# Kernel tuning notes

Measured on AMD Instinct MI355X. Metric: run time of the kernel, lower is better.

The kernel has to match this reference:

```python
import jax, jax.numpy as jnp
import numpy as np

EPS = 1e-5

def _ln(x, g, b):
    m = x.mean(-1, keepdims=True)
    v = ((x - m) ** 2).mean(-1, keepdims=True)
    return (x - m) / jnp.sqrt(v + EPS) * g + b


def setup_inputs() -> dict:
    key = jax.random.key(0)
    B, S = 16, 512
    H, dh = 16, 64            # num_head, head_size
    D = H * dh                # 1024
    NB = 2                    # num_blocks
    L = 2                     # attention_mlp_layers
    ks = jax.random.split(key, 16)
    sc = 1.0 / np.sqrt(D)
    inp = {
        'inputs': jax.random.normal(ks[0], (B, S, D), jnp.float32),
        'Wq': jax.random.normal(ks[1], (NB, H, D, dh), jnp.float32) * sc,
        'Wk': jax.random.normal(ks[2], (NB, H, D, dh), jnp.float32) * sc,
        'Wv': jax.random.normal(ks[3], (NB, H, D, dh), jnp.float32) * sc,
        'qg': jnp.ones((NB, dh), jnp.float32), 'qb': jnp.zeros((NB, dh), jnp.float32),
        'kg': jnp.ones((NB, dh), jnp.float32), 'kb': jnp.zeros((NB, dh), jnp.float32),
        'vg': jnp.ones((NB, dh), jnp.float32), 'vb': jnp.zeros((NB, dh), jnp.float32),
        'l0g': jnp.ones((NB, D), jnp.float32), 'l0b': jnp.zeros((NB, D), jnp.float32),
        'l1g': jnp.ones((NB, D), jnp.float32), 'l1b': jnp.zeros((NB, D), jnp.float32),
        'mW': jax.random.normal(ks[4], (NB, L, D, D), jnp.float32) * sc,
        'mB': jnp.zeros((NB, L, D), jnp.float32),
    }
    return inp


def reference(inputs, Wq, Wk, Wv, qg, qb, kg, kb, vg, vb, l0g, l0b, l1g, l1b, mW, mB):
    B, S, D = inputs.shape
    NB, H, _, dh = Wq.shape
    L = mW.shape[1]
    scale = 1.0 / np.sqrt(dh)  # source divides by sqrt(value_dim/n_heads)
    x = inputs
    maps = []
    for i in range(NB):
        # per-head projections: torch repeats batch over heads then bmm with [H,D,dh]
        q = jnp.einsum('bsd,hde->bhse', x, Wq[i])
        k = jnp.einsum('bsd,hde->bhse', x, Wk[i])
        v = jnp.einsum('bsd,hde->bhse', x, Wv[i])
        qn = _ln(q, qg[i], qb[i])
        kn = _ln(k, kg[i], kb[i])
        vn = _ln(v, vg[i], vb[i])
        # NOTE: the source applies NO softmax — raw scaled scores are used.
        attn = jnp.einsum('bhse,bhte->bhst', qn, kn) * scale
        o = jnp.einsum('bhst,bhte->bhse', attn, vn)
        # torch layout is (H*B, S, S) with head-major ordering
        maps.append(jnp.transpose(attn, (1, 0, 2, 3)).reshape(H * B, S, S))
        # concat heads on last dim (head-major split/cat == bhse -> bshe reshape)
        o = jnp.transpose(o, (0, 2, 1, 3)).reshape(B, S, D)
        new = _ln(x + o, l0g[i], l0b[i])  # dropout is identity in eval
        h = new
        for l in range(L):
            h = jax.nn.relu(h @ mW[i, l] + mB[i, l])
        x = _ln(new + h, l1g[i], l1b[i])
    return x, jnp.stack(maps)
```

## Files before the change

### kernel.cpp

```cpp
#include <hip/hip_runtime.h>
#include <cstddef>
#include <cstdint>

#define B_   16
#define S_   512
#define D_   1024
#define H_   16
#define DH_  64
#define BS_  8192
#define EPS_ 1e-5f

typedef __attribute__((ext_vector_type(8))) short bf16x8;
typedef __attribute__((ext_vector_type(4))) short s16x4;
typedef __attribute__((ext_vector_type(4))) float f32x4;

__device__ __forceinline__ unsigned short f2bf(float f) {
    unsigned int u = __builtin_bit_cast(unsigned int, f);
    u = (u + 0x7FFFu + ((u >> 16) & 1u)) >> 16;
    return (unsigned short)u;
}
__device__ __forceinline__ float bf2f(unsigned short h) {
    unsigned int u = ((unsigned int)h) << 16;
    return __builtin_bit_cast(float, u);
}
__device__ __forceinline__ void splitbf(float v, short& hi, short& lo) {
    unsigned short h = f2bf(v);
    float r = v - bf2f(h);
    hi = (short)h;
    lo = (short)f2bf(r);
}

__device__ __forceinline__ void gload16(const void* g, void* l) {
    __builtin_amdgcn_global_load_lds(
        (const __attribute__((address_space(1))) unsigned int*)g,
        (__attribute__((address_space(3))) unsigned int*)l, 16, 0, 0);
}


__device__ __forceinline__ void mainloop128(
    const short* __restrict__ Ah, const short* __restrict__ Al,
    const short* __restrict__ Bh, const short* __restrict__ Bl,
    int nkt, short* lds, f32x4 acc[4][4])
{
    const int t = threadIdx.x;
    const int wid = t >> 6, lane = t & 63;
    short* LAh = lds;
    short* LAl = lds + 4096;
    short* LBh = lds + 8192;
    short* LBl = lds + 12288;
    const int fa = (wid >> 1) * 4;
    const int fb = (wid & 1) * 4;
    for (int kt = 0; kt < nkt; ++kt) {
        const size_t go = (size_t)kt * 4096 + (size_t)t * 8;
        gload16(Ah + go,        LAh + t * 8);
        gload16(Ah + go + 2048, LAh + t * 8 + 2048);
        gload16(Al + go,        LAl + t * 8);
        gload16(Al + go + 2048, LAl + t * 8 + 2048);
        gload16(Bh + go,        LBh + t * 8);
        gload16(Bh + go + 2048, LBh + t * 8 + 2048);
        gload16(Bl + go,        LBl + t * 8);
        gload16(Bl + go + 2048, LBl + t * 8 + 2048);
        asm volatile("s_waitcnt vmcnt(0)" ::: "memory");
        __syncthreads();
        bf16x8 aH[4], aL[4];
        #pragma unroll
        for (int fm = 0; fm < 4; ++fm) {
            aH[fm] = *(const bf16x8*)(LAh + (fa + fm) * 512 + lane * 8);
            aL[fm] = *(const bf16x8*)(LAl + (fa + fm) * 512 + lane * 8);
        }
        #pragma unroll
        for (int fn = 0; fn < 4; ++fn) {
            bf16x8 bH = *(const bf16x8*)(LBh + (fb + fn) * 512 + lane * 8);
            bf16x8 bL = *(const bf16x8*)(LBl + (fb + fn) * 512 + lane * 8);
            #pragma unroll
            for (int fm = 0; fm < 4; ++fm) {
                acc[fm][fn] = __builtin_amdgcn_mfma_f32_16x16x32_bf16(aH[fm], bH, acc[fm][fn], 0, 0, 0);
                acc[fm][fn] = __builtin_amdgcn_mfma_f32_16x16x32_bf16(aH[fm], bL, acc[fm][fn], 0, 0, 0);
                acc[fm][fn] = __builtin_amdgcn_mfma_f32_16x16x32_bf16(aL[fm], bH, acc[fm][fn], 0, 0, 0);
            }
        }
        __syncthreads();
    }
}

__global__ __launch_bounds__(256, 3) void proj_kernel(
    const short* __restrict__ XPh, const short* __restrict__ XPl,
    const short* __restrict__ WTh, const short* __restrict__ WTl,
    const float* __restrict__ gq, const float* __restrict__ bq,
    const float* __restrict__ gk, const float* __restrict__ bk,
    const float* __restrict__ gv, const float* __restrict__ bv,
    short* __restrict__ QPh, short* __restrict__ QPl,
    short* __restrict__ KPh, short* __restrict__ KPl,
    short* __restrict__ VPh, short* __restrict__ VPl)
{
    __shared__ __align__(16) short lds[16384];
    const int mt = blockIdx.x, nt = blockIdx.y;
    f32x4 acc[4][4] = {};
    mainloop128(XPh + (size_t)mt * 131072, XPl + (size_t)mt * 131072,
                WTh + (size_t)nt * 131072, WTl + (size_t)nt * 131072,
                32, lds, acc);
    const int t = threadIdx.x, wid = t >> 6, lane = t & 63;
    const int g = lane >> 4, li = lane & 15;
    const int wm = (wid >> 1) * 64, wn = (wid & 1) * 64;
    const int n0 = nt * 128 + wn;
    const int qkv = n0 >> 10;
    const int h = (n0 >> 6) & 15;
    const float* gam = qkv == 0 ? gq : (qkv == 1 ? gk : gv);
    const float* bet = qkv == 0 ? bq : (qkv == 1 ? bk : bv);
    float gm[4], bt[4];
    #pragma unroll
    for (int fn = 0; fn < 4; ++fn) { gm[fn] = gam[fn * 16 + li]; bt[fn] = bet[fn * 16 + li]; }
    #pragma unroll
    for (int fm = 0; fm < 4; ++fm) {
        #pragma unroll
        for (int r = 0; r < 4; ++r) {
            float s = acc[fm][0][r] + acc[fm][1][r] + acc[fm][2][r] + acc[fm][3][r];
            s += __shfl_xor(s, 1, 64); s += __shfl_xor(s, 2, 64);
            s += __shfl_xor(s, 4, 64); s += __shfl_xor(s, 8, 64);
            const float mean = s * (1.f / 64.f);
            float q = 0.f;
            #pragma unroll
            for (int fn = 0; fn < 4; ++fn) { const float d = acc[fm][fn][r] - mean; q += d * d; }
            q += __shfl_xor(q, 1, 64); q += __shfl_xor(q, 2, 64);
            q += __shfl_xor(q, 4, 64); q += __shfl_xor(q, 8, 64);
            const float rstd = rsqrtf(q * (1.f / 64.f) + EPS_);
            const int m = mt * 128 + wm + fm * 16 + g * 4 + r;
            const int b = m >> 9, srow = m & 511;
            const int z = b * 16 + h;
            #pragma unroll
            for (int fn = 0; fn < 4; ++fn) {
                const float val = (acc[fm][fn][r] - mean) * rstd * gm[fn] + bt[fn];
                short hi, lo; splitbf(val, hi, lo);
                const int e = fn * 16 + li;
                if (qkv == 2) {
                    const size_t o = (size_t)z * 32768 + (size_t)srow * 64 + e;
                    VPh[o] = hi; VPl[o] = lo;
                } else {
                    const size_t o = ((size_t)((z * 4 + (srow >> 7)) * 2 + (e >> 5))) * 4096
                                   + ((((srow >> 4) & 7) * 4 + ((e >> 3) & 3)) * 16 + (srow & 15)) * 8 + (e & 7);
                    if (qkv == 0) { QPh[o] = hi; QPl[o] = lo; }
                    else          { KPh[o] = hi; KPl[o] = lo; }
                }
            }
        }
    }
}

template<int MODE>
__global__ __launch_bounds__(256, 3) void mlp_kernel(
    const short* __restrict__ Ah, const short* __restrict__ Al,
    const short* __restrict__ Bh, const short* __restrict__ Bl,
    const float* __restrict__ bias,
    short* __restrict__ OPh, short* __restrict__ OPl,
    float* __restrict__ OF)
{
    __shared__ __align__(16) short lds[16384];
    const int mt = blockIdx.x, nt = blockIdx.y;
    f32x4 acc[4][4] = {};
    mainloop128(Ah + (size_t)mt * 131072, Al + (size_t)mt * 131072,
                Bh + (size_t)nt * 131072, Bl + (size_t)nt * 131072, 32, lds, acc);
    const int t = threadIdx.x, wid = t >> 6, lane = t & 63;
    const int g = lane >> 4, li = lane & 15;
    const int wm = (wid >> 1) * 64, wn = (wid & 1) * 64;
    float bb[4];
    #pragma unroll
    for (int fn = 0; fn < 4; ++fn) bb[fn] = bias[nt * 128 + wn + fn * 16 + li];
    #pragma unroll
    for (int fm = 0; fm < 4; ++fm) {
        #pragma unroll
        for (int r = 0; r < 4; ++r) {
            const int m = mt * 128 + wm + fm * 16 + g * 4 + r;
            #pragma unroll
            for (int fn = 0; fn < 4; ++fn) {
                const int n = nt * 128 + wn + fn * 16 + li;
                float v = acc[fm][fn][r] + bb[fn];
                v = v > 0.f ? v : 0.f;
                if (MODE == 1) {
                    short hi, lo; splitbf(v, hi, lo);
                    const size_t o = ((size_t)mt * 32 + (n >> 5)) * 4096
                                   + ((((m >> 4) & 7) * 4 + ((n >> 3) & 3)) * 16 + (m & 15)) * 8 + (n & 7);
                    OPh[o] = hi; OPl[o] = lo;
                } else {
                    OF[(size_t)m * 1024 + n] = v;
                }
            }
        }
    }
}

__global__ __launch_bounds__(256, 3) void scores_kernel(
    const short* __restrict__ QPh, const short* __restrict__ QPl,
    const short* __restrict__ KPh, const short* __restrict__ KPl,
    float* __restrict__ mapsi)
{
    __shared__ __align__(16) short lds[16384];
    const int mt = blockIdx.x, nt = blockIdx.y, z = blockIdx.z;
    f32x4 acc[4][4] = {};
    const size_t ab = (size_t)(z * 4 + mt) * 8192;
    const size_t bb2 = (size_t)(z * 4 + nt) * 8192;
    mainloop128(QPh + ab, QPl + ab, KPh + bb2, KPl + bb2, 2, lds, acc);
    const int t = threadIdx.x, wid = t >> 6, lane = t & 63;
    const int g = lane >> 4, li = lane & 15;
    const int wm = (wid >> 1) * 64, wn = (wid & 1) * 64;
    const int zp = ((z & 15) << 4) | (z >> 4);
    float* P = mapsi + (size_t)zp * (S_ * S_);
    #pragma unroll
    for (int fm = 0; fm < 4; ++fm) {
        #pragma unroll
        for (int r = 0; r < 4; ++r) {
            const int srow = mt * 128 + wm + fm * 16 + g * 4 + r;
            #pragma unroll
            for (int fn = 0; fn < 4; ++fn) {
                const int tc = nt * 128 + wn + fn * 16 + li;
                P[(size_t)srow * 512 + tc] = acc[fm][fn][r] * 0.125f;
            }
        }
    }
}

__global__ __launch_bounds__(256, 3) void o_kernel(
    const float* __restrict__ maps, const short* __restrict__ VTh,
    const short* __restrict__ VTl, float* __restrict__ O)
{
    __shared__ __align__(16) short lds[12288];
    const int bid = blockIdx.x;
    const int xcd = bid & 7, tt = bid >> 3;
    const int mt = tt & 3;
    const int z = (tt >> 2) * 8 + xcd;
    const int zp = ((z & 15) << 4) | (z >> 4);
    const float* P = maps + (size_t)zp * (S_ * S_);
    const short* Bh = VTh + (size_t)z * 32768;
    const short* Bl = VTl + (size_t)z * 32768;
    short* LAh = lds;
    short* LAl = lds + 4096;
    short* LBh = lds + 8192;
    short* LBl = lds + 10240;
    const int t = threadIdx.x, wid = t >> 6, lane = t & 63;
    const int fa = (wid >> 1) * 4, fb = (wid & 1) * 2;
    f32x4 acc[4][2] = {};
    for (int kt = 0; kt < 16; ++kt) {
        gload16(Bh + (size_t)kt * 2048 + t * 8, LBh + t * 8);
        gload16(Bl + (size_t)kt * 2048 + t * 8, LBl + t * 8);
        #pragma unroll
        for (int cc = 0; cc < 2; ++cc) {
            const int c = t + cc * 256;
            const int srow = mt * 128 + (c >> 6) * 16 + (c & 15);
            const int k0 = kt * 32 + ((c >> 4) & 3) * 8;
            const float* src = P + (size_t)srow * 512 + k0;
            const f32x4 v0 = *(const f32x4*)(src);
            const f32x4 v1 = *(const f32x4*)(src + 4);
            bf16x8 h8, l8;
            #pragma unroll
            for (int j = 0; j < 4; ++j) {
                short hi, lo;
                splitbf(v0[j], hi, lo); h8[j] = hi;     l8[j] = lo;
                splitbf(v1[j], hi, lo); h8[4 + j] = hi; l8[4 + j] = lo;
            }
            *(bf16x8*)(LAh + c * 8) = h8;
            *(bf16x8*)(LAl + c * 8) = l8;
        }
        asm volatile("s_waitcnt vmcnt(0)" ::: "memory");
        __syncthreads();
        bf16x8 aH[4], aL[4];
        #pragma unroll
        for (int fm = 0; fm < 4; ++fm) {
            aH[fm] = *(const bf16x8*)(LAh + (fa + fm) * 512 + lane * 8);
            aL[fm] = *(const bf16x8*)(LAl + (fa + fm) * 512 + lane * 8);
        }
        #pragma unroll
        for (int fn = 0; fn < 2; ++fn) {
            bf16x8 bH = *(const bf16x8*)(LBh + (fb + fn) * 512 + lane * 8);
            bf16x8 bL = *(const bf16x8*)(LBl + (fb + fn) * 512 + lane * 8);
            #pragma unroll
            for (int fm = 0; fm < 4; ++fm) {
                acc[fm][fn] = __builtin_amdgcn_mfma_f32_16x16x32_bf16(aH[fm], bH, acc[fm][fn], 0, 0, 0);
                acc[fm][fn] = __builtin_amdgcn_mfma_f32_16x16x32_bf16(aH[fm], bL, acc[fm][fn], 0, 0, 0);
                acc[fm][fn] = __builtin_amdgcn_mfma_f32_16x16x32_bf16(aL[fm], bH, acc[fm][fn], 0, 0, 0);
            }
        }
        __syncthreads();
    }
    const int b = z >> 4, h = z & 15;
    const int g = lane >> 4, li = lane & 15;
    #pragma unroll
    for (int fm = 0; fm < 4; ++fm) {
        #pragma unroll
        for (int r = 0; r < 4; ++r) {
            const int srow = mt * 128 + (wid >> 1) * 64 + fm * 16 + g * 4 + r;
            #pragma unroll
            for (int fn = 0; fn < 2; ++fn) {
                const int e = (wid & 1) * 32 + fn * 16 + li;
                O[((size_t)b * 512 + srow) * 1024 + h * 64 + e] = acc[fm][fn][r];
            }
        }
    }
}

__global__ __launch_bounds__(256) void vt_kernel(
    const short* __restrict__ VPh, const short* __restrict__ VPl,
    short* __restrict__ VTh, short* __restrict__ VTl)
{
    const int z = blockIdx.x, kt = blockIdx.y;
    __shared__ __align__(16) short Th[32][80];
    __shared__ __align__(16) short Tl[32][80];
    const int t = threadIdx.x;
    {
        const int row = t >> 3;
        const int e0 = (t & 7) * 8;
        const size_t src = (size_t)z * 32768 + (size_t)(kt * 32 + row) * 64 + e0;
        *(bf16x8*)&Th[row][e0] = *(const bf16x8*)(VPh + src);
        *(bf16x8*)&Tl[row][e0] = *(const bf16x8*)(VPl + src);
    }
    __syncthreads();
    {
        const int c = t;
        const int fn = c >> 6, kc = (c >> 4) & 3, n16 = c & 15;
        const int e = fn * 16 + n16;
        bf16x8 h8, l8;
        #pragma unroll
        for (int j = 0; j < 8; ++j) {
            h8[j] = Th[kc * 8 + j][e];
            l8[j] = Tl[kc * 8 + j][e];
        }
        const size_t o = ((size_t)z * 16 + kt) * 2048 + (size_t)c * 8;
        *(bf16x8*)(VTh + o) = h8;
        *(bf16x8*)(VTl + o) = l8;
    }
}

__global__ __launch_bounds__(256) void ln_add_kernel(
    const float* __restrict__ A, const float* __restrict__ C,
    const float* __restrict__ g, const float* __restrict__ bb,
    float* __restrict__ out, short* __restrict__ Ph, short* __restrict__ Pl)
{
    const int m = blockIdx.x;
    const int t = threadIdx.x;
    const int wave = t >> 6, lane = t & 63;
    __shared__ float red1[4];
    __shared__ float red2[4];
    const int k0 = t * 4;
    const f32x4 va = *(const f32x4*)(A + (size_t)m * 1024 + k0);
    const f32x4 vc = *(const f32x4*)(C + (size_t)m * 1024 + k0);
    f32x4 v = va + vc;
    float s = v[0] + v[1] + v[2] + v[3];
    #pragma unroll
    for (int off = 32; off > 0; off >>= 1) s += __shfl_xor(s, off, 64);
    if (lane == 0) red1[wave] = s;
    __syncthreads();
    const float mean = (red1[0] + red1[1] + red1[2] + red1[3]) * (1.f / 1024.f);
    float q = 0.f;
    #pragma unroll
    for (int j = 0; j < 4; ++j) { const float d = v[j] - mean; q += d * d; }
    #pragma unroll
    for (int off = 32; off > 0; off >>= 1) q += __shfl_xor(q, off, 64);
    if (lane == 0) red2[wave] = q;
    __syncthreads();
    const float rstd = rsqrtf((red2[0] + red2[1] + red2[2] + red2[3]) * (1.f / 1024.f) + EPS_);
    const f32x4 gg = *(const f32x4*)(g + k0);
    const f32x4 bv = *(const f32x4*)(bb + k0);
    f32x4 o;
    s16x4 hi4, lo4;
    #pragma unroll
    for (int j = 0; j < 4; ++j) {
        o[j] = (v[j] - mean) * rstd * gg[j] + bv[j];
        short hi, lo; splitbf(o[j], hi, lo);
        hi4[j] = hi; lo4[j] = lo;
    }
    *(f32x4*)(out + (size_t)m * 1024 + k0) = o;
    const size_t po = ((size_t)(m >> 7) * 32 + (k0 >> 5)) * 4096
                    + ((((m >> 4) & 7) * 4 + ((k0 >> 3) & 3)) * 16 + (m & 15)) * 8 + (k0 & 7);
    *(s16x4*)(Ph + po) = hi4;
    *(s16x4*)(Pl + po) = lo4;
}

__global__ __launch_bounds__(256) void cvt_kernel(
    const float* __restrict__ X, short* __restrict__ Ph, short* __restrict__ Pl)
{
    const int m = blockIdx.x;
    const int t = threadIdx.x;
    const int k0 = t * 4;
    const f32x4 v = *(const f32x4*)(X + (size_t)m * 1024 + k0);
    s16x4 hi4, lo4;
    #pragma unroll
    for (int j = 0; j < 4; ++j) { short hi, lo; splitbf(v[j], hi, lo); hi4[j] = hi; lo4[j] = lo; }
    const size_t po = ((size_t)(m >> 7) * 32 + (k0 >> 5)) * 4096
                    + ((((m >> 4) & 7) * 4 + ((k0 >> 3) & 3)) * 16 + (m & 15)) * 8 + (k0 & 7);
    *(s16x4*)(Ph + po) = hi4;
    *(s16x4*)(Pl + po) = lo4;
}

__global__ __launch_bounds__(256) void prep_wqkv_kernel(
    const float* __restrict__ Wq, const float* __restrict__ Wk,
    const float* __restrict__ Wv, short* __restrict__ WTh, short* __restrict__ WTl)
{
    const int nt = blockIdx.x;
    const int kt = blockIdx.y;
    const int qkv = nt >> 3;
    const float* W = qkv == 0 ? Wq : (qkv == 1 ? Wk : Wv);
    const int t = threadIdx.x;
    short* oh = WTh + ((size_t)nt * 32 + kt) * 4096;
    short* ol = WTl + ((size_t)nt * 32 + kt) * 4096;
    #pragma unroll
    for (int cc = 0; cc < 2; ++cc) {
        const int c = t + cc * 256;
        const int nloc = (c >> 6) * 16 + (c & 15);
        const int nq = (nt & 7) * 128 + nloc;
        const int h = nq >> 6, e = nq & 63;
        const int d0 = kt * 32 + ((c >> 4) & 3) * 8;
        bf16x8 h8, l8;
        #pragma unroll
        for (int j = 0; j < 8; ++j) {
            const float v = W[((size_t)h * 1024 + d0 + j) * 64 + e];
            short hi, lo; splitbf(v, hi, lo);
            h8[j] = hi; l8[j] = lo;
        }
        *(bf16x8*)(oh + c * 8) = h8;
        *(bf16x8*)(ol + c * 8) = l8;
    }
}

__global__ __launch_bounds__(256) void prep_mw_kernel(
    const float* __restrict__ Wm, short* __restrict__ Mh, short* __restrict__ Ml)
{
    const int nt = blockIdx.x;
    const int kt = blockIdx.y;
    const int l  = blockIdx.z;
    const float* W = Wm + (size_t)l * 1048576;
    short* oh = Mh + (size_t)l * 1048576 + ((size_t)nt * 32 + kt) * 4096;
    short* ol = Ml + (size_t)l * 1048576 + ((size_t)nt * 32 + kt) * 4096;
    const int t = threadIdx.x;
    #pragma unroll
    for (int cc = 0; cc < 2; ++cc) {
        const int c = t + cc * 256;
        const int n = nt * 128 + (c >> 6) * 16 + (c & 15);
        const int k0 = kt * 32 + ((c >> 4) & 3) * 8;
        bf16x8 h8, l8;
        #pragma unroll
        for (int j = 0; j < 8; ++j) {
            const float v = W[(size_t)(k0 + j) * 1024 + n];
            short hi, lo; splitbf(v, hi, lo);
            h8[j] = hi; l8[j] = lo;
        }
        *(bf16x8*)(oh + c * 8) = h8;
        *(bf16x8*)(ol + c * 8) = l8;
    }
}

extern "C" void kernel_launch(void* const* d_in, const int* in_sizes, int n_in,
                              void* d_out, int out_size, void* d_ws, size_t ws_size,
                              hipStream_t stream)
{
    const float* inputs = (const float*)d_in[0];
    const float* Wq  = (const float*)d_in[1];
    const float* Wk  = (const float*)d_in[2];
    const float* Wv  = (const float*)d_in[3];
    const float* qg  = (const float*)d_in[4];
    const float* qb  = (const float*)d_in[5];
    const float* kg  = (const float*)d_in[6];
    const float* kb  = (const float*)d_in[7];
    const float* vg  = (const float*)d_in[8];
    const float* vb  = (const float*)d_in[9];
    const float* l0g = (const float*)d_in[10];
    const float* l0b = (const float*)d_in[11];
    const float* l1g = (const float*)d_in[12];
    const float* l1b = (const float*)d_in[13];
    const float* mW  = (const float*)d_in[14];
    const float* mB  = (const float*)d_in[15];

    float* xout = (float*)d_out;
    float* maps = xout + (size_t)BS_ * D_;

    char* ws = (char*)d_ws;
    short* XPh = (short*)(ws);
    short* XPl = (short*)(ws + 16777216);
    short* QPh = (short*)(ws + 33554432);
    short* QPl = (short*)(ws + 50331648);
    short* KPh = (short*)(ws + 67108864);
    short* KPl = (short*)(ws + 83886080);
    float* NEW = (float*)(ws + 100663296);
    short* VPh = (short*)(ws + 100663296);
    short* VPl = (short*)(ws + 117440512);
    float* OF  = (float*)(ws + 134217728);
    short* WTh = (short*)(ws + 167772160);
    short* WTl = (short*)(ws + 174063616);
    short* MWh = (short*)(ws + 180355072);
    short* MWl = (short*)(ws + 184549376);
    short* VTh = XPh;
    short* VTl = XPl;

    const dim3 blk(256);
    for (int i = 0; i < 2; ++i) {
        const float* xin = (i == 0) ? inputs : xout;
        float* mapsi = maps + (size_t)i * H_ * B_ * S_ * S_;

        if (i == 0)
            cvt_kernel<<<dim3(BS_), blk, 0, stream>>>(inputs, XPh, XPl);

        prep_wqkv_kernel<<<dim3(24, 32), blk, 0, stream>>>(
            Wq + (size_t)i * H_ * D_ * DH_, Wk + (size_t)i * H_ * D_ * DH_,
            Wv + (size_t)i * H_ * D_ * DH_, WTh, WTl);
        prep_mw_kernel<<<dim3(8, 32, 2), blk, 0, stream>>>(
            mW + (size_t)i * 2 * D_ * D_, MWh, MWl);

        proj_kernel<<<dim3(64, 24), blk, 0, stream>>>(
            XPh, XPl, WTh, WTl,
            qg + i * DH_, qb + i * DH_, kg + i * DH_, kb + i * DH_,
            vg + i * DH_, vb + i * DH_,
            QPh, QPl, KPh, KPl, VPh, VPl);

        vt_kernel<<<dim3(256, 16), blk, 0, stream>>>(VPh, VPl, VTh, VTl);

        scores_kernel<<<dim3(4, 4, 256), blk, 0, stream>>>(QPh, QPl, KPh, KPl, mapsi);

        o_kernel<<<dim3(1024), blk, 0, stream>>>(mapsi, VTh, VTl, OF);

        ln_add_kernel<<<dim3(BS_), blk, 0, stream>>>(
            xin, OF, l0g + i * D_, l0b + i * D_, NEW, KPh, KPl);

        mlp_kernel<1><<<dim3(64, 8), blk, 0, stream>>>(
            KPh, KPl, MWh, MWl, mB + (size_t)(i * 2 + 0) * D_, QPh, QPl, (float*)nullptr);
        mlp_kernel<2><<<dim3(64, 8), blk, 0, stream>>>(
            QPh, QPl, MWh + 1048576, MWl + 1048576, mB + (size_t)(i * 2 + 1) * D_,
            (short*)nullptr, (short*)nullptr, OF);

        ln_add_kernel<<<dim3(BS_), blk, 0, stream>>>(
            NEW, OF, l1g + i * D_, l1b + i * D_, xout, XPh, XPl);
    }
}
```

Measured before the change: 1.576 ms.

## Compute attention output via Q(KᵀV) reassociation instead of reading score maps

Because no softmax is applied, the output is computed as Q·(KᵀV·scale) per head in a new kernel. This replaces the kernel that re-read the full fp32 score maps and multiplied them by V, removing a large memory-bound pass. The score maps are still written, now with nontemporal stores, and the maps output region serves as scratch for row-major K/V and their transposes before scores_kernel overwrites it. Projection and MLP grids are remapped to a 1D launch with an XCD-aware block swizzle. The cost is an extra K write, an extra transpose kernel and scratch aliasing that depends on the launch order.

```diff
diff --git a/kernel.cpp b/kernel.cpp
--- a/kernel.cpp
+++ b/kernel.cpp
@@ -91,10 +91,13 @@
     const float* __restrict__ gv, const float* __restrict__ bv,
     short* __restrict__ QPh, short* __restrict__ QPl,
     short* __restrict__ KPh, short* __restrict__ KPl,
-    short* __restrict__ VPh, short* __restrict__ VPl)
+    short* __restrict__ KRMh, short* __restrict__ KRMl,
+    short* __restrict__ VRMh, short* __restrict__ VRMl)
 {
     __shared__ __align__(16) short lds[16384];
-    const int mt = blockIdx.x, nt = blockIdx.y;
+    const int f  = blockIdx.x;
+    const int nf = (f & 7) * 192 + (f >> 3);
+    const int mt = nf & 63, nt = nf >> 6;
     f32x4 acc[4][4] = {};
     mainloop128(XPh + (size_t)mt * 131072, XPl + (size_t)mt * 131072,
                 WTh + (size_t)nt * 131072, WTl + (size_t)nt * 131072,
@@ -134,12 +137,16 @@
                 const int e = fn * 16 + li;
                 if (qkv == 2) {
                     const size_t o = (size_t)z * 32768 + (size_t)srow * 64 + e;
-                    VPh[o] = hi; VPl[o] = lo;
+                    VRMh[o] = hi; VRMl[o] = lo;
                 } else {
                     const size_t o = ((size_t)((z * 4 + (srow >> 7)) * 2 + (e >> 5))) * 4096
                                    + ((((srow >> 4) & 7) * 4 + ((e >> 3) & 3)) * 16 + (srow & 15)) * 8 + (e & 7);
                     if (qkv == 0) { QPh[o] = hi; QPl[o] = lo; }
-                    else          { KPh[o] = hi; KPl[o] = lo; }
+                    else {
+                        KPh[o] = hi; KPl[o] = lo;
+                        const size_t o2 = (size_t)z * 32768 + (size_t)srow * 64 + e;
+                        KRMh[o2] = hi; KRMl[o2] = lo;
+                    }
                 }
             }
         }
@@ -155,7 +162,9 @@
     float* __restrict__ OF)
 {
     __shared__ __align__(16) short lds[16384];
-    const int mt = blockIdx.x, nt = blockIdx.y;
+    const int f  = blockIdx.x;
+    const int nf = (f & 7) * 64 + (f >> 3);
+    const int mt = nf & 63, nt = nf >> 6;
     f32x4 acc[4][4] = {};
     mainloop128(Ah + (size_t)mt * 131072, Al + (size_t)mt * 131072,
                 Bh + (size_t)nt * 131072, Bl + (size_t)nt * 131072, 32, lds, acc);
@@ -212,93 +221,108 @@
             #pragma unroll
             for (int fn = 0; fn < 4; ++fn) {
                 const int tc = nt * 128 + wn + fn * 16 + li;
-                P[(size_t)srow * 512 + tc] = acc[fm][fn][r] * 0.125f;
-            }
-        }
-    }
-}
-
-__global__ __launch_bounds__(256, 3) void o_kernel(
-    const float* __restrict__ maps, const short* __restrict__ VTh,
-    const short* __restrict__ VTl, float* __restrict__ O)
-{
-    __shared__ __align__(16) short lds[12288];
-    const int bid = blockIdx.x;
-    const int xcd = bid & 7, tt = bid >> 3;
-    const int mt = tt & 3;
-    const int z = (tt >> 2) * 8 + xcd;
-    const int zp = ((z & 15) << 4) | (z >> 4);
-    const float* P = maps + (size_t)zp * (S_ * S_);
-    const short* Bh = VTh + (size_t)z * 32768;
-    const short* Bl = VTl + (size_t)z * 32768;
-    short* LAh = lds;
-    short* LAl = lds + 4096;
-    short* LBh = lds + 8192;
-    short* LBl = lds + 10240;
+                __builtin_nontemporal_store(acc[fm][fn][r] * 0.125f,
+                                            P + (size_t)srow * 512 + tc);
+            }
+        }
+    }
+}
+
+__global__ __launch_bounds__(256) void kvo2_kernel(
+    const short* __restrict__ VTKh, const short* __restrict__ VTKl,
+    const short* __restrict__ VTVh, const short* __restrict__ VTVl,
+    const short* __restrict__ QPh, const short* __restrict__ QPl,
+    float* __restrict__ O)
+{
+    __shared__ __align__(16) short kvt[8192];
+    __shared__ __align__(16) short qs[16384];
+    const int z = blockIdx.x;
     const int t = threadIdx.x, wid = t >> 6, lane = t & 63;
-    const int fa = (wid >> 1) * 4, fb = (wid & 1) * 2;
-    f32x4 acc[4][2] = {};
+    const int g = lane >> 4, li = lane & 15;
+
+    f32x4 acc[4] = {};
+    const size_t zb = (size_t)z * 32768;
     for (int kt = 0; kt < 16; ++kt) {
-        gload16(Bh + (size_t)kt * 2048 + t * 8, LBh + t * 8);
-        gload16(Bl + (size_t)kt * 2048 + t * 8, LBl + t * 8);
-        #pragma unroll
-        for (int cc = 0; cc < 2; ++cc) {
-            const int c = t + cc * 256;
-            const int srow = mt * 128 + (c >> 6) * 16 + (c & 15);
-            const int k0 = kt * 32 + ((c >> 4) & 3) * 8;
-            const float* src = P + (size_t)srow * 512 + k0;
-            const f32x4 v0 = *(const f32x4*)(src);
-            const f32x4 v1 = *(const f32x4*)(src + 4);
-            bf16x8 h8, l8;
-            #pragma unroll
-            for (int j = 0; j < 4; ++j) {
-                short hi, lo;
-                splitbf(v0[j], hi, lo); h8[j] = hi;     l8[j] = lo;
-                splitbf(v1[j], hi, lo); h8[4 + j] = hi; l8[4 + j] = lo;
-            }
-            *(bf16x8*)(LAh + c * 8) = h8;
-            *(bf16x8*)(LAl + c * 8) = l8;
-        }
+        const size_t tb = zb + (size_t)kt * 2048;
+        const bf16x8 aH = *(const bf16x8*)(VTKh + tb + wid * 512 + lane * 8);
+        const bf16x8 aL = *(const bf16x8*)(VTKl + tb + wid * 512 + lane * 8);
+        #pragma unroll
+        for (int fn = 0; fn < 4; ++fn) {
+            const bf16x8 bH = *(const bf16x8*)(VTVh + tb + fn * 512 + lane * 8);
+            const bf16x8 bL = *(const bf16x8*)(VTVl + tb + fn * 512 + lane * 8);
+            acc[fn] = __builtin_amdgcn_mfma_f32_16x16x32_bf16(aH, bH, acc[fn], 0, 0, 0);
+            acc[fn] = __builtin_amdgcn_mfma_f32_16x16x32_bf16(aH, bL, acc[fn], 0, 0, 0);
+            acc[fn] = __builtin_amdgcn_mfma_f32_16x16x32_bf16(aL, bH, acc[fn], 0, 0, 0);
+        }
+    }
+    #pragma unroll
+    for (int fn = 0; fn < 4; ++fn) {
+        #pragma unroll
+        for (int r = 0; r < 4; ++r) {
+            const int e1 = wid * 16 + g * 4 + r;
+            const int e2 = fn * 16 + li;
+            short hi, lo; splitbf(acc[fn][r] * 0.125f, hi, lo);
+            const int a = (e1 >> 5) * 2048 + (e2 >> 4) * 512
+                        + ((((e1 >> 3) & 3) * 16) + (e2 & 15)) * 8 + (e1 & 7);
+            kvt[a] = hi; kvt[4096 + a] = lo;
+        }
+    }
+    __syncthreads();
+
+    const int b = z >> 4, h = z & 15;
+    const int fa = (wid >> 1) * 4, fbn = (wid & 1) * 2;
+    for (int mt = 0; mt < 4; ++mt) {
+        __syncthreads();
+        const size_t qb = (size_t)(z * 4 + mt) * 8192;
+        gload16(QPh + qb + t * 8,        qs + t * 8);
+        gload16(QPh + qb + t * 8 + 2048, qs + t * 8 + 2048);
+        gload16(QPh + qb + t * 8 + 4096, qs + t * 8 + 4096);
+        gload16(QPh + qb + t * 8 + 6144, qs + t * 8 + 6144);
+        gload16(QPl + qb + t * 8,        qs + 8192 + t * 8);
+        gload16(QPl + qb + t * 8 + 2048, qs + 8192 + t * 8 + 2048);
+        gload16(QPl + qb + t * 8 + 4096, qs + 8192 + t * 8 + 4096);
+        gload16(QPl + qb + t * 8 + 6144, qs + 8192 + t * 8 + 6144);
         asm volatile("s_waitcnt vmcnt(0)" ::: "memory");
         __syncthreads();
-        bf16x8 aH[4], aL[4];
+        f32x4 a3[4][2] = {};
+        #pragma unroll
+        for (int kt2 = 0; kt2 < 2; ++kt2) {
+            bf16x8 aH[4], aL[4];
+            #pragma unroll
+            for (int fm = 0; fm < 4; ++fm) {
+                aH[fm] = *(const bf16x8*)(qs + kt2 * 4096 + (fa + fm) * 512 + lane * 8);
+                aL[fm] = *(const bf16x8*)(qs + 8192 + kt2 * 4096 + (fa + fm) * 512 + lane * 8);
+            }
+            #pragma unroll
+            for (int fnb = 0; fnb < 2; ++fnb) {
+                const bf16x8 bH = *(const bf16x8*)(kvt + kt2 * 2048 + (fbn + fnb) * 512 + lane * 8);
+                const bf16x8 bL = *(const bf16x8*)(kvt + 4096 + kt2 * 2048 + (fbn + fnb) * 512 + lane * 8);
+                #pragma unroll
+                for (int fm = 0; fm < 4; ++fm) {
+                    a3[fm][fnb] = __builtin_amdgcn_mfma_f32_16x16x32_bf16(aH[fm], bH, a3[fm][fnb], 0, 0, 0);
+                    a3[fm][fnb] = __builtin_amdgcn_mfma_f32_16x16x32_bf16(aH[fm], bL, a3[fm][fnb], 0, 0, 0);
+                    a3[fm][fnb] = __builtin_amdgcn_mfma_f32_16x16x32_bf16(aL[fm], bH, a3[fm][fnb], 0, 0, 0);
+                }
+            }
+        }
         #pragma unroll
         for (int fm = 0; fm < 4; ++fm) {
-            aH[fm] = *(const bf16x8*)(LAh + (fa + fm) * 512 + lane * 8);
-            aL[fm] = *(const bf16x8*)(LAl + (fa + fm) * 512 + lane * 8);
-        }
-        #pragma unroll
-        for (int fn = 0; fn < 2; ++fn) {
-            bf16x8 bH = *(const bf16x8*)(LBh + (fb + fn) * 512 + lane * 8);
-            bf16x8 bL = *(const bf16x8*)(LBl + (fb + fn) * 512 + lane * 8);
-            #pragma unroll
-            for (int fm = 0; fm < 4; ++fm) {
-                acc[fm][fn] = __builtin_amdgcn_mfma_f32_16x16x32_bf16(aH[fm], bH, acc[fm][fn], 0, 0, 0);
-                acc[fm][fn] = __builtin_amdgcn_mfma_f32_16x16x32_bf16(aH[fm], bL, acc[fm][fn], 0, 0, 0);
-                acc[fm][fn] = __builtin_amdgcn_mfma_f32_16x16x32_bf16(aL[fm], bH, acc[fm][fn], 0, 0, 0);
-            }
-        }
-        __syncthreads();
-    }
-    const int b = z >> 4, h = z & 15;
-    const int g = lane >> 4, li = lane & 15;
-    #pragma unroll
-    for (int fm = 0; fm < 4; ++fm) {
-        #pragma unroll
-        for (int r = 0; r < 4; ++r) {
-            const int srow = mt * 128 + (wid >> 1) * 64 + fm * 16 + g * 4 + r;
-            #pragma unroll
-            for (int fn = 0; fn < 2; ++fn) {
-                const int e = (wid & 1) * 32 + fn * 16 + li;
-                O[((size_t)b * 512 + srow) * 1024 + h * 64 + e] = acc[fm][fn][r];
+            #pragma unroll
+            for (int r = 0; r < 4; ++r) {
+                const int s = mt * 128 + (wid >> 1) * 64 + fm * 16 + g * 4 + r;
+                #pragma unroll
+                for (int fnb = 0; fnb < 2; ++fnb) {
+                    const int e2 = (fbn + fnb) * 16 + li;
+                    O[((size_t)b * 512 + s) * 1024 + h * 64 + e2] = a3[fm][fnb][r];
+                }
             }
         }
     }
 }
 
 __global__ __launch_bounds__(256) void vt_kernel(
-    const short* __restrict__ VPh, const short* __restrict__ VPl,
-    short* __restrict__ VTh, short* __restrict__ VTl)
+    const short* __restrict__ Sh, const short* __restrict__ Sl,
+    short* __restrict__ Dh, short* __restrict__ Dl)
 {
     const int z = blockIdx.x, kt = blockIdx.y;
     __shared__ __align__(16) short Th[32][80];
@@ -308,8 +332,8 @@
         const int row = t >> 3;
         const int e0 = (t & 7) * 8;
         const size_t src = (size_t)z * 32768 + (size_t)(kt * 32 + row) * 64 + e0;
-        *(bf16x8*)&Th[row][e0] = *(const bf16x8*)(VPh + src);
-        *(bf16x8*)&Tl[row][e0] = *(const bf16x8*)(VPl + src);
+        *(bf16x8*)&Th[row][e0] = *(const bf16x8*)(Sh + src);
+        *(bf16x8*)&Tl[row][e0] = *(const bf16x8*)(Sl + src);
     }
     __syncthreads();
     {
@@ -323,8 +347,8 @@
             l8[j] = Tl[kc * 8 + j][e];
         }
         const size_t o = ((size_t)z * 16 + kt) * 2048 + (size_t)c * 8;
-        *(bf16x8*)(VTh + o) = h8;
-        *(bf16x8*)(VTl + o) = l8;
+        *(bf16x8*)(Dh + o) = h8;
+        *(bf16x8*)(Dl + o) = l8;
     }
 }
 
@@ -478,20 +502,25 @@
     short* KPh = (short*)(ws + 67108864);
     short* KPl = (short*)(ws + 83886080);
     float* NEW = (float*)(ws + 100663296);
-    short* VPh = (short*)(ws + 100663296);
-    short* VPl = (short*)(ws + 117440512);
     float* OF  = (float*)(ws + 134217728);
     short* WTh = (short*)(ws + 167772160);
     short* WTl = (short*)(ws + 174063616);
     short* MWh = (short*)(ws + 180355072);
     short* MWl = (short*)(ws + 184549376);
-    short* VTh = XPh;
-    short* VTl = XPl;
 
     const dim3 blk(256);
     for (int i = 0; i < 2; ++i) {
         const float* xin = (i == 0) ? inputs : xout;
         float* mapsi = maps + (size_t)i * H_ * B_ * S_ * S_;
+
+        short* KRMh = (short*)mapsi;
+        short* KRMl = KRMh + 8388608;
+        short* VRMh = KRMh + 16777216;
+        short* VRMl = KRMh + 25165824;
+        short* VTKh = KRMh + 33554432;
+        short* VTKl = KRMh + 41943040;
+        short* VTVh = KRMh + 50331648;
+        short* VTVl = KRMh + 58720256;
 
         if (i == 0)
             cvt_kernel<<<dim3(BS_), blk, 0, stream>>>(inputs, XPh, XPl);
@@ -502,24 +531,26 @@
         prep_mw_kernel<<<dim3(8, 32, 2), blk, 0, stream>>>(
             mW + (size_t)i * 2 * D_ * D_, MWh, MWl);
 
-        proj_kernel<<<dim3(64, 24), blk, 0, stream>>>(
+        proj_kernel<<<dim3(1536), blk, 0, stream>>>(
             XPh, XPl, WTh, WTl,
             qg + i * DH_, qb + i * DH_, kg + i * DH_, kb + i * DH_,
             vg + i * DH_, vb + i * DH_,
-            QPh, QPl, KPh, KPl, VPh, VPl);
-
-        vt_kernel<<<dim3(256, 16), blk, 0, stream>>>(VPh, VPl, VTh, VTl);
+            QPh, QPl, KPh, KPl, KRMh, KRMl, VRMh, VRMl);
+
+        vt_kernel<<<dim3(256, 16), blk, 0, stream>>>(KRMh, KRMl, VTKh, VTKl);
+        vt_kernel<<<dim3(256, 16), blk, 0, stream>>>(VRMh, VRMl, VTVh, VTVl);
+
+        kvo2_kernel<<<dim3(256), blk, 0, stream>>>(
+            VTKh, VTKl, VTVh, VTVl, QPh, QPl, OF);
 
         scores_kernel<<<dim3(4, 4, 256), blk, 0, stream>>>(QPh, QPl, KPh, KPl, mapsi);
-
-        o_kernel<<<dim3(1024), blk, 0, stream>>>(mapsi, VTh, VTl, OF);
 
         ln_add_kernel<<<dim3(BS_), blk, 0, stream>>>(
             xin, OF, l0g + i * D_, l0b + i * D_, NEW, KPh, KPl);
 
-        mlp_kernel<1><<<dim3(64, 8), blk, 0, stream>>>(
+        mlp_kernel<1><<<dim3(512), blk, 0, stream>>>(
             KPh, KPl, MWh, MWl, mB + (size_t)(i * 2 + 0) * D_, QPh, QPl, (float*)nullptr);
-        mlp_kernel<2><<<dim3(64, 8), blk, 0, stream>>>(
+        mlp_kernel<2><<<dim3(512), blk, 0, stream>>>(
             QPh, QPl, MWh + 1048576, MWl + 1048576, mB + (size_t)(i * 2 + 1) * D_,
             (short*)nullptr, (short*)nullptr, OF);
 
```

New measurement: 1.597 ms. About the same (+1.3%).
